# Performance work log

Hardware: AMD Instinct MI355X
Metric: run time of the kernel (lower is better)

## Reference

```python
import jax, jax.numpy as jnp
import numpy as np

# weight_dict {0:1,1:1,2:1,3:1} with similarity_pyramid=True -> w_l = 1/2^l
WEIGHTS = [1.0, 0.5, 0.25, 0.125]
WINS = [9, 9, 7, 5]
NCC_FACTOR = 100.0
N_LOSSES = 2  # ['mse', 'ncc']


def _sliding_sum(x, win, axis):
    """Box (ones-kernel) sliding-window sum along one axis, 'same' output via
    zero padding of win//2 on each side -- separable equivalent of the dense
    ones-kernel conv in the original NCC_loss."""
    pad = win // 2
    pw = [(0, 0)] * x.ndim
    pw[axis] = (pad + 1, pad)  # extra leading zero so cumsum diff gives window sums
    c = jnp.cumsum(jnp.pad(x, pw), axis=axis)
    n = x.shape[axis]
    hi = jax.lax.slice_in_dim(c, win, win + n, axis=axis)
    lo = jax.lax.slice_in_dim(c, 0, n, axis=axis)
    return hi - lo


def _box_sum(x, win):
    # x: [B,1,H,W]; 2D box filter == separable 1D sliding sums
    return _sliding_sum(_sliding_sum(x, win, 2), win, 3)


def _ncc_loss(y_pred, y_true, win):
    Ii, Ji = y_true, y_pred
    ws = float(win * win)
    I_sum = _box_sum(Ii, win)
    J_sum = _box_sum(Ji, win)
    I2_sum = _box_sum(Ii * Ii, win)
    J2_sum = _box_sum(Ji * Ji, win)
    IJ_sum = _box_sum(Ii * Ji, win)
    u_I = I_sum / ws
    u_J = J_sum / ws
    cross = IJ_sum - u_J * I_sum - u_I * J_sum + u_I * u_J * ws
    I_var = I2_sum - 2.0 * u_I * I_sum + u_I * u_I * ws
    J_var = J2_sum - 2.0 * u_J * J_sum + u_J * u_J * ws
    cc = cross * cross / (I_var * J_var + 1e-8)
    return -jnp.sum(jnp.mean(cc, axis=0)) / NCC_FACTOR


def _l2_loss(inp, tgt):
    # sum over spatial dims, mean over batch & channel
    return jnp.mean(jnp.sum((inp - tgt) ** 2, axis=(2, 3)))


def _hier_loss(y_hats, y):
    total = jnp.zeros((), dtype=y.dtype)
    levels = []
    for l, yh in enumerate(y_hats):
        if yh.shape == y.shape:
            yt = y
        else:
            # F.interpolate bilinear align_corners=False == half-pixel linear resize
            yt = jax.image.resize(y, yh.shape, method='linear', antialias=False)
        w = WEIGHTS[l]
        ll = (w * _l2_loss(yh, yt) + w * _ncc_loss(yh, yt, WINS[l])) / N_LOSSES
        levels.append(ll)
        total = total + ll
    return total, levels


def setup_inputs() -> dict:
    key = jax.random.key(0)
    ks = jax.random.split(key, 5)
    return {
        'y_hat_0': jax.random.uniform(ks[0], (32, 1, 512, 512), dtype=jnp.float32),
        'y_hat_1': jax.random.uniform(ks[1], (32, 1, 256, 256), dtype=jnp.float32),
        'y_hat_2': jax.random.uniform(ks[2], (32, 1, 128, 128), dtype=jnp.float32),
        'y_hat_3': jax.random.uniform(ks[3], (32, 1, 64, 64), dtype=jnp.float32),
        'y': jax.random.uniform(ks[4], (32, 1, 512, 512), dtype=jnp.float32),
    }


def reference(y_hat_0, y_hat_1, y_hat_2, y_hat_3, y):
    total, levels = _hier_loss([y_hat_0, y_hat_1, y_hat_2, y_hat_3], y)
    return (total, *levels)
```

## Files before the change

### kernel.cpp

```cpp
#include <hip/hip_runtime.h>

#define NT 256

#define SMEM_FLOATS 12096

template<int W, int H, int WIN, int SCALE, int CW, int RCHUNK>
__device__ void level_block(const float* __restrict__ yh,
                            const float* __restrict__ y,
                            float* smem, int sub, float* ws_acc, int level)
{
    constexpr int HW = WIN / 2;
    constexpr int RW = CW + 2 * HW;

    float* ring = smem;
    float* rawI = ring + WIN * 5 * CW;
    float* rawJ = rawI + RW;
    float* red  = rawJ + RW;

    constexpr int STRIPS = W / CW;
    constexpr int CHUNKS = H / RCHUNK;
    int b     = sub / (STRIPS * CHUNKS);
    int rem   = sub % (STRIPS * CHUNKS);
    int chunk = rem / STRIPS;
    int strip = rem % STRIPS;
    int r0 = chunk * RCHUNK, r1 = r0 + RCHUNK;
    int c0 = strip * CW;

    const float* Jimg = yh + (size_t)b * (size_t)W * (size_t)H;
    const float* Yimg = y  + (size_t)b * 512 * 512;

    int t = threadIdx.x;

    float vI = 0.f, vJ = 0.f, vII = 0.f, vJJ = 0.f, vIJ = 0.f;
    float l2acc = 0.f, ccacc = 0.f;

    for (int r = r0 - HW; r < r1 + HW; ++r) {
        if (r >= 0 && r < H) {
            for (int i = t; i < RW; i += NT) {
                int j = c0 - HW + i;
                float I = 0.f, J = 0.f;
                if (j >= 0 && j < W) {
                    J = Jimg[(size_t)r * W + j];
                    if (SCALE == 1) {
                        I = Yimg[(size_t)r * 512 + j];
                    } else {
                        constexpr int OFF = (SCALE - 2) / 2;
                        int rr = SCALE * r + OFF;
                        int cc = SCALE * j + OFF;
                        const float* p = Yimg + (size_t)rr * 512 + cc;
                        I = 0.25f * (p[0] + p[1] + p[512] + p[513]);
                    }
                    if (j >= c0 && j < c0 + CW && r >= r0 && r < r1) {
                        float d = J - I;
                        l2acc += d * d;
                    }
                }
                rawI[i] = I;
                rawJ[i] = J;
            }
            __syncthreads();
            if (t < CW) {
                float sI = 0.f, sJ = 0.f, sII = 0.f, sJJ = 0.f, sIJ = 0.f;
#pragma unroll
                for (int k = 0; k < WIN; ++k) {
                    float I = rawI[t + k];
                    float J = rawJ[t + k];
                    sI += I; sJ += J;
                    sII += I * I; sJJ += J * J; sIJ += I * J;
                }
                int slot = r % WIN;
                float* rp = ring + (size_t)slot * 5 * CW;
                rp[0 * CW + t] = sI;
                rp[1 * CW + t] = sJ;
                rp[2 * CW + t] = sII;
                rp[3 * CW + t] = sJJ;
                rp[4 * CW + t] = sIJ;
                vI += sI; vJ += sJ; vII += sII; vJJ += sJJ; vIJ += sIJ;
            }
            __syncthreads();
        }
        int yrow = r - HW;
        if (yrow >= r0 && yrow < r1 && t < CW) {
            const float wsq = (float)(WIN * WIN);
            float cross = vIJ - vI * vJ / wsq;
            float Ivar  = vII - vI * vI / wsq;
            float Jvar  = vJJ - vJ * vJ / wsq;
            float cc = cross * cross / (Ivar * Jvar + 1e-8f);
            ccacc += cc;
            int rl = yrow - HW;
            if (rl >= 0) {
                int slot = rl % WIN;
                float* rp = ring + (size_t)slot * 5 * CW;
                vI  -= rp[0 * CW + t];
                vJ  -= rp[1 * CW + t];
                vII -= rp[2 * CW + t];
                vJJ -= rp[3 * CW + t];
                vIJ -= rp[4 * CW + t];
            }
        }
    }

    __syncthreads();
#pragma unroll
    for (int off = 32; off > 0; off >>= 1) {
        l2acc += __shfl_down(l2acc, off);
        ccacc += __shfl_down(ccacc, off);
    }
    int wave = t >> 6, lane = t & 63;
    if (lane == 0) { red[wave] = l2acc; red[8 + wave] = ccacc; }
    __syncthreads();
    if (t == 0) {
        float l2t = 0.f, cct = 0.f;
#pragma unroll
        for (int w = 0; w < NT / 64; ++w) { l2t += red[w]; cct += red[8 + w]; }
        atomicAdd(&ws_acc[level], l2t);
        atomicAdd(&ws_acc[4 + level], cct);
    }
}

__global__ __launch_bounds__(NT)
void hier_loss_kernel(const float* __restrict__ yh0, const float* __restrict__ yh1,
                      const float* __restrict__ yh2, const float* __restrict__ yh3,
                      const float* __restrict__ y, float* ws_acc)
{
    __shared__ float smem[SMEM_FLOATS];
    int bid = blockIdx.x;
    if (bid < 512) {
        level_block<512, 512, 9, 1, 256, 64>(yh0, y, smem, bid, ws_acc, 0);
    } else if (bid < 640) {
        level_block<256, 256, 9, 2, 256, 64>(yh1, y, smem, bid - 512, ws_acc, 1);
    } else if (bid < 704) {
        level_block<128, 128, 7, 4, 128, 64>(yh2, y, smem, bid - 640, ws_acc, 2);
    } else {
        level_block<64, 64, 5, 8, 64, 64>(yh3, y, smem, bid - 704, ws_acc, 3);
    }
}

__global__ void hier_finalize_kernel(const float* __restrict__ ws_acc, float* __restrict__ out)
{
    if (blockIdx.x == 0 && threadIdx.x == 0) {
        const float wts[4] = {1.0f, 0.5f, 0.25f, 0.125f};
        float total = 0.f;
#pragma unroll
        for (int l = 0; l < 4; ++l) {
            float l2 = ws_acc[l] / 32.0f;
            float ncc = -ws_acc[4 + l] / (32.0f * 100.0f);
            float ll = wts[l] * (l2 + ncc) * 0.5f;
            out[1 + l] = ll;
            total += ll;
        }
        out[0] = total;
    }
}

extern "C" void kernel_launch(void* const* d_in, const int* in_sizes, int n_in,
                              void* d_out, int out_size, void* d_ws, size_t ws_size,
                              hipStream_t stream)
{
    const float* yh0 = (const float*)d_in[0];
    const float* yh1 = (const float*)d_in[1];
    const float* yh2 = (const float*)d_in[2];
    const float* yh3 = (const float*)d_in[3];
    const float* y   = (const float*)d_in[4];
    float* ws_acc = (float*)d_ws;
    float* out = (float*)d_out;

    hipMemsetAsync(ws_acc, 0, 8 * sizeof(float), stream);
    hier_loss_kernel<<<736, NT, 0, stream>>>(yh0, yh1, yh2, yh3, y, ws_acc);
    hier_finalize_kernel<<<1, 64, 0, stream>>>(ws_acc, out);
}
```

Baseline: 109.9 us.

## Restructure NCC loss to per-wave strips with register ring buffers

Each wave now processes its own 64-column by 32-row tile, so block-wide __syncthreads become wave-level barriers. The vertical sliding-window ring moves from shared memory into fully unrolled register arrays. Reductions are spread across 32 atomic slots per accumulator to reduce contention. The costs are higher register pressure, more halo reloads from the smaller row chunks, and many more, smaller work units.

```diff
diff --git a/kernel.cpp b/kernel.cpp
--- a/kernel.cpp
+++ b/kernel.cpp
@@ -1,120 +1,143 @@
 #include <hip/hip_runtime.h>
 
 #define NT 256
-
-#define SMEM_FLOATS 12096
-
-template<int W, int H, int WIN, int SCALE, int CW, int RCHUNK>
-__device__ void level_block(const float* __restrict__ yh,
-                            const float* __restrict__ y,
-                            float* smem, int sub, float* ws_acc, int level)
+#define RCHUNK 32
+#define NSLOT 32
+
+
+__device__ __forceinline__ void wave_fence_after_write() {
+    __builtin_amdgcn_wave_barrier();
+    asm volatile("s_waitcnt lgkmcnt(0)" ::: "memory");
+    __builtin_amdgcn_sched_barrier(0);
+}
+__device__ __forceinline__ void wave_fence_after_read() {
+    __builtin_amdgcn_wave_barrier();
+    __builtin_amdgcn_sched_barrier(0);
+}
+
+template<int W, int H, int WIN, int SCALE>
+__device__ void level_wave(const float* __restrict__ yh,
+                           const float* __restrict__ y,
+                           int sub, float* __restrict__ ws_acc, int level,
+                           float* rawI, float* rawJ)
 {
     constexpr int HW = WIN / 2;
-    constexpr int RW = CW + 2 * HW;
-
-    float* ring = smem;
-    float* rawI = ring + WIN * 5 * CW;
-    float* rawJ = rawI + RW;
-    float* red  = rawJ + RW;
-
-    constexpr int STRIPS = W / CW;
+    constexpr int RW = 64 + 2 * HW;
+    constexpr int T  = RCHUNK + 2 * HW;
+    constexpr int G  = (T + WIN - 1) / WIN;
+    constexpr float INV_WS = 1.0f / (float)(WIN * WIN);
+
+    constexpr int STRIPS = W / 64;
     constexpr int CHUNKS = H / RCHUNK;
     int b     = sub / (STRIPS * CHUNKS);
     int rem   = sub % (STRIPS * CHUNKS);
     int chunk = rem / STRIPS;
     int strip = rem % STRIPS;
-    int r0 = chunk * RCHUNK, r1 = r0 + RCHUNK;
-    int c0 = strip * CW;
-
-    const float* Jimg = yh + (size_t)b * (size_t)W * (size_t)H;
+    int r0 = chunk * RCHUNK;
+    int c0 = strip * 64;
+
+    const float* Jimg = yh + (size_t)b * W * H;
     const float* Yimg = y  + (size_t)b * 512 * 512;
 
-    int t = threadIdx.x;
-
+    int l = threadIdx.x & 63;
+
+    float ringI[WIN], ringJ[WIN], ringII[WIN], ringJJ[WIN], ringIJ[WIN];
+#pragma unroll
+    for (int k = 0; k < WIN; ++k) {
+        ringI[k] = 0.f; ringJ[k] = 0.f; ringII[k] = 0.f; ringJJ[k] = 0.f; ringIJ[k] = 0.f;
+    }
     float vI = 0.f, vJ = 0.f, vII = 0.f, vJJ = 0.f, vIJ = 0.f;
     float l2acc = 0.f, ccacc = 0.f;
 
-    for (int r = r0 - HW; r < r1 + HW; ++r) {
-        if (r >= 0 && r < H) {
-            for (int i = t; i < RW; i += NT) {
-                int j = c0 - HW + i;
+    for (int g = 0; g < G; ++g) {
+#pragma unroll
+        for (int u = 0; u < WIN; ++u) {
+            int rr = g * WIN + u;
+            int r  = r0 - HW + rr;
+            bool rin = (rr < T) && (r >= 0) && (r < H);
+
+            {
+                int j = c0 - HW + l;
                 float I = 0.f, J = 0.f;
-                if (j >= 0 && j < W) {
+                if (rin && j >= 0 && j < W) {
                     J = Jimg[(size_t)r * W + j];
                     if (SCALE == 1) {
                         I = Yimg[(size_t)r * 512 + j];
                     } else {
                         constexpr int OFF = (SCALE - 2) / 2;
-                        int rr = SCALE * r + OFF;
-                        int cc = SCALE * j + OFF;
-                        const float* p = Yimg + (size_t)rr * 512 + cc;
+                        const float* p = Yimg + (size_t)(SCALE * r + OFF) * 512 + (SCALE * j + OFF);
                         I = 0.25f * (p[0] + p[1] + p[512] + p[513]);
                     }
-                    if (j >= c0 && j < c0 + CW && r >= r0 && r < r1) {
-                        float d = J - I;
-                        l2acc += d * d;
+                }
+                rawI[l] = I;
+                rawJ[l] = J;
+                if (l < RW - 64) {
+                    int j2 = j + 64;
+                    float I2 = 0.f, J2 = 0.f;
+                    if (rin && j2 < W) {
+                        J2 = Jimg[(size_t)r * W + j2];
+                        if (SCALE == 1) {
+                            I2 = Yimg[(size_t)r * 512 + j2];
+                        } else {
+                            constexpr int OFF = (SCALE - 2) / 2;
+                            const float* p = Yimg + (size_t)(SCALE * r + OFF) * 512 + (SCALE * j2 + OFF);
+                            I2 = 0.25f * (p[0] + p[1] + p[512] + p[513]);
+                        }
                     }
+                    rawI[l + 64] = I2;
+                    rawJ[l + 64] = J2;
                 }
-                rawI[i] = I;
-                rawJ[i] = J;
-            }
-            __syncthreads();
-            if (t < CW) {
-                float sI = 0.f, sJ = 0.f, sII = 0.f, sJJ = 0.f, sIJ = 0.f;
-#pragma unroll
-                for (int k = 0; k < WIN; ++k) {
-                    float I = rawI[t + k];
-                    float J = rawJ[t + k];
-                    sI += I; sJ += J;
-                    sII += I * I; sJJ += J * J; sIJ += I * J;
-                }
-                int slot = r % WIN;
-                float* rp = ring + (size_t)slot * 5 * CW;
-                rp[0 * CW + t] = sI;
-                rp[1 * CW + t] = sJ;
-                rp[2 * CW + t] = sII;
-                rp[3 * CW + t] = sJJ;
-                rp[4 * CW + t] = sIJ;
-                vI += sI; vJ += sJ; vII += sII; vJJ += sJJ; vIJ += sIJ;
-            }
-            __syncthreads();
+            }
+            wave_fence_after_write();
+
+            float sI = 0.f, sJ = 0.f, sII = 0.f, sJJ = 0.f, sIJ = 0.f;
+            float Ic = 0.f, Jc = 0.f;
+#pragma unroll
+            for (int k = 0; k < WIN; ++k) {
+                float I = rawI[l + k];
+                float J = rawJ[l + k];
+                if (k == HW) { Ic = I; Jc = J; }
+                sI += I; sJ += J;
+                sII = fmaf(I, I, sII);
+                sJJ = fmaf(J, J, sJJ);
+                sIJ = fmaf(I, J, sIJ);
+            }
+            wave_fence_after_read();
+
+            if (rr >= HW && rr < RCHUNK + HW) {
+                float d = Jc - Ic;
+                l2acc = fmaf(d, d, l2acc);
+            }
+
+            ringI[u] = sI; ringJ[u] = sJ; ringII[u] = sII; ringJJ[u] = sJJ; ringIJ[u] = sIJ;
+            vI += sI; vJ += sJ; vII += sII; vJJ += sJJ; vIJ += sIJ;
+
+            if (rr >= 2 * HW && rr < T) {
+                float cross = fmaf(-(vI * vJ), INV_WS, vIJ);
+                float Iv    = fmaf(-(vI * vI), INV_WS, vII);
+                float Jv    = fmaf(-(vJ * vJ), INV_WS, vJJ);
+                float cc = (cross * cross) / (Iv * Jv + 1e-8f);
+                ccacc += cc;
+                constexpr int dummy = 0; (void)dummy;
+                const int us = (u + 1) % WIN;
+                vI  -= ringI[us];
+                vJ  -= ringJ[us];
+                vII -= ringII[us];
+                vJJ -= ringJJ[us];
+                vIJ -= ringIJ[us];
+            }
         }
-        int yrow = r - HW;
-        if (yrow >= r0 && yrow < r1 && t < CW) {
-            const float wsq = (float)(WIN * WIN);
-            float cross = vIJ - vI * vJ / wsq;
-            float Ivar  = vII - vI * vI / wsq;
-            float Jvar  = vJJ - vJ * vJ / wsq;
-            float cc = cross * cross / (Ivar * Jvar + 1e-8f);
-            ccacc += cc;
-            int rl = yrow - HW;
-            if (rl >= 0) {
-                int slot = rl % WIN;
-                float* rp = ring + (size_t)slot * 5 * CW;
-                vI  -= rp[0 * CW + t];
-                vJ  -= rp[1 * CW + t];
-                vII -= rp[2 * CW + t];
-                vJJ -= rp[3 * CW + t];
-                vIJ -= rp[4 * CW + t];
-            }
-        }
-    }
-
-    __syncthreads();
+    }
+
 #pragma unroll
     for (int off = 32; off > 0; off >>= 1) {
         l2acc += __shfl_down(l2acc, off);
         ccacc += __shfl_down(ccacc, off);
     }
-    int wave = t >> 6, lane = t & 63;
-    if (lane == 0) { red[wave] = l2acc; red[8 + wave] = ccacc; }
-    __syncthreads();
-    if (t == 0) {
-        float l2t = 0.f, cct = 0.f;
-#pragma unroll
-        for (int w = 0; w < NT / 64; ++w) { l2t += red[w]; cct += red[8 + w]; }
-        atomicAdd(&ws_acc[level], l2t);
-        atomicAdd(&ws_acc[4 + level], cct);
+    if (l == 0) {
+        int slot = sub & (NSLOT - 1);
+        atomicAdd(&ws_acc[(level * 2 + 0) * NSLOT + slot], l2acc);
+        atomicAdd(&ws_acc[(level * 2 + 1) * NSLOT + slot], ccacc);
     }
 }
 
@@ -123,30 +146,39 @@
                       const float* __restrict__ yh2, const float* __restrict__ yh3,
                       const float* __restrict__ y, float* ws_acc)
 {
-    __shared__ float smem[SMEM_FLOATS];
-    int bid = blockIdx.x;
-    if (bid < 512) {
-        level_block<512, 512, 9, 1, 256, 64>(yh0, y, smem, bid, ws_acc, 0);
-    } else if (bid < 640) {
-        level_block<256, 256, 9, 2, 256, 64>(yh1, y, smem, bid - 512, ws_acc, 1);
-    } else if (bid < 704) {
-        level_block<128, 128, 7, 4, 128, 64>(yh2, y, smem, bid - 640, ws_acc, 2);
+    __shared__ float smem[4][2][80];
+    int wave = threadIdx.x >> 6;
+    float* rawI = &smem[wave][0][0];
+    float* rawJ = &smem[wave][1][0];
+
+    int wid = blockIdx.x * (NT / 64) + wave;
+    if (wid < 4096) {
+        level_wave<512, 512, 9, 1>(yh0, y, wid, ws_acc, 0, rawI, rawJ);
+    } else if (wid < 5120) {
+        level_wave<256, 256, 9, 2>(yh1, y, wid - 4096, ws_acc, 1, rawI, rawJ);
+    } else if (wid < 5376) {
+        level_wave<128, 128, 7, 4>(yh2, y, wid - 5120, ws_acc, 2, rawI, rawJ);
     } else {
-        level_block<64, 64, 5, 8, 64, 64>(yh3, y, smem, bid - 704, ws_acc, 3);
+        level_wave<64, 64, 5, 8>(yh3, y, wid - 5376, ws_acc, 3, rawI, rawJ);
     }
 }
 
 __global__ void hier_finalize_kernel(const float* __restrict__ ws_acc, float* __restrict__ out)
 {
-    if (blockIdx.x == 0 && threadIdx.x == 0) {
+    if (threadIdx.x == 0 && blockIdx.x == 0) {
         const float wts[4] = {1.0f, 0.5f, 0.25f, 0.125f};
         float total = 0.f;
 #pragma unroll
-        for (int l = 0; l < 4; ++l) {
-            float l2 = ws_acc[l] / 32.0f;
-            float ncc = -ws_acc[4 + l] / (32.0f * 100.0f);
-            float ll = wts[l] * (l2 + ncc) * 0.5f;
-            out[1 + l] = ll;
+        for (int lv = 0; lv < 4; ++lv) {
+            float l2s = 0.f, ccs = 0.f;
+            for (int s = 0; s < NSLOT; ++s) {
+                l2s += ws_acc[(lv * 2 + 0) * NSLOT + s];
+                ccs += ws_acc[(lv * 2 + 1) * NSLOT + s];
+            }
+            float l2  = l2s / 32.0f;
+            float ncc = -ccs / (32.0f * 100.0f);
+            float ll  = wts[lv] * (l2 + ncc) * 0.5f;
+            out[1 + lv] = ll;
             total += ll;
         }
         out[0] = total;
@@ -165,7 +197,7 @@
     float* ws_acc = (float*)d_ws;
     float* out = (float*)d_out;
 
-    hipMemsetAsync(ws_acc, 0, 8 * sizeof(float), stream);
-    hier_loss_kernel<<<736, NT, 0, stream>>>(yh0, yh1, yh2, yh3, y, ws_acc);
+    hipMemsetAsync(ws_acc, 0, 8 * NSLOT * sizeof(float), stream);
+    hier_loss_kernel<<<5440 / (NT / 64), NT, 0, stream>>>(yh0, yh1, yh2, yh3, y, ws_acc);
     hier_finalize_kernel<<<1, 64, 0, stream>>>(ws_acc, out);
 }
```

Result: slower. 121.9 us (+10.9%).
